# Optimization experiments

Measured on AMD Instinct MI355X. Metric: run time of the kernel, lower is better.

Reference implementation:

```python
import jax, jax.numpy as jnp
import numpy as np

STRIDES = (8.0, 16.0, 32.0)


def _decode_level(feat, W, b, stride, level):
    # feat: [bs, C, ny, nx]; W: [85, C]; b: [85]
    bs, _, ny, nx = feat.shape
    # 1x1 conv == channel contraction; output laid out as [bs, ny, nx, 85]
    p = jnp.einsum('bchw,oc->bhwo', feat, W) + b
    y = jax.nn.sigmoid(p)
    xv = jnp.arange(nx, dtype=y.dtype)            # broadcasts over last spatial dim
    yv = jnp.arange(ny, dtype=y.dtype)[:, None]   # broadcasts over row dim
    power = jnp.asarray(2.0 ** level, dtype=y.dtype)
    d = (y[..., :4] * 2.0) ** 2 * power           # dx1, dy1, dx2, dy2
    x1 = (xv + 1.0 - d[..., 0]) * stride
    y1 = (yv + 1.0 - d[..., 1]) * stride
    x2 = (xv + d[..., 2]) * stride
    y2 = (yv + d[..., 3]) * stride
    # xyxy -> xywh
    box = jnp.stack([(x1 + x2) * 0.5, (y1 + y2) * 0.5, x2 - x1, y2 - y1], axis=-1)
    out = jnp.concatenate([box, y[..., 4:]], axis=-1)  # [bs, ny, nx, 85]
    return out.reshape(bs, ny * nx, out.shape[-1])


def setup_inputs() -> dict:
    key = jax.random.key(0)
    ks = jax.random.split(key, 9)
    f32 = jnp.float32
    return {
        'x0': jax.random.normal(ks[0], (16, 256, 80, 80), dtype=f32),
        'x1': jax.random.normal(ks[1], (16, 512, 40, 40), dtype=f32),
        'x2': jax.random.normal(ks[2], (16, 1024, 20, 20), dtype=f32),
        'W0': jax.random.normal(ks[3], (85, 256), dtype=f32) * 0.05,
        'b0': jax.random.normal(ks[4], (85,), dtype=f32) * 0.05,
        'W1': jax.random.normal(ks[5], (85, 512), dtype=f32) * 0.05,
        'b1': jax.random.normal(ks[6], (85,), dtype=f32) * 0.05,
        'W2': jax.random.normal(ks[7], (85, 1024), dtype=f32) * 0.05,
        'b2': jax.random.normal(ks[8], (85,), dtype=f32) * 0.05,
    }


def reference(x0, x1, x2, W0, b0, W1, b1, W2, b2):
    feats = (x0, x1, x2)
    Ws = (W0, W1, W2)
    bs_ = (b0, b1, b2)
    z = [_decode_level(feats[i], Ws[i], bs_[i], STRIDES[i], i) for i in range(3)]
    return jnp.concatenate(z, axis=1)  # [bs, 8400, 85]
```

## Files before the change

### kernel.cpp

```cpp
#include <hip/hip_runtime.h>
#include <cstdint>


typedef __attribute__((ext_vector_type(8))) short bf16x8;
typedef __attribute__((ext_vector_type(4))) float f32x4;

constexpr int KS0 = 8, KS1 = 16, KS2 = 32;
constexpr int F0 = 6 * KS0, F1 = 6 * KS1, F2 = 6 * KS2;
constexpr int FOFF0 = 0, FOFF1 = F0, FOFF2 = F0 + F1;
constexpr int NFRAG = F0 + F1 + F2;
constexpr size_t BIAS_OFF = 0;
constexpr size_t BPK_OFF  = 1152;
constexpr size_t WS_NEED  = BPK_OFF + (size_t)NFRAG * 64 * 16;

__device__ __forceinline__ unsigned short f2bf(float f) {
    union { float f; unsigned u; } v; v.f = f;
    unsigned r = v.u + 0x7FFF + ((v.u >> 16) & 1);
    return (unsigned short)(r >> 16);
}

__global__ __launch_bounds__(256) void prep_pack(
    const float* __restrict__ W0, const float* __restrict__ W1,
    const float* __restrict__ W2,
    const float* __restrict__ b0, const float* __restrict__ b1,
    const float* __restrict__ b2,
    unsigned char* __restrict__ ws)
{
    int t = blockIdx.x * 256 + threadIdx.x;
    if (t < 288) {
        int lvl = t / 96, o = t % 96;
        const float* bp = (lvl == 0) ? b0 : (lvl == 1) ? b1 : b2;
        ((float*)(ws + BIAS_OFF))[t] = (o < 85) ? bp[o] : 0.0f;
    }
    if (t >= NFRAG * 64) return;
    int frag = t >> 6, l = t & 63;
    int C; const float* W; int f;
    if (frag < FOFF1)      { C = 256;  W = W0; f = frag;         }
    else if (frag < FOFF2) { C = 512;  W = W1; f = frag - FOFF1; }
    else                   { C = 1024; W = W2; f = frag - FOFF2; }
    int ks = f / 6, n = f % 6;
    int o  = n * 16 + (l & 15);
    int c0 = ks * 32 + (l >> 4) * 8;
    bf16x8 r;
#pragma unroll
    for (int e = 0; e < 8; ++e)
        r[e] = (o < 85) ? (short)f2bf(W[(size_t)o * C + c0 + e]) : (short)0;
    ((bf16x8*)(ws + BPK_OFF))[frag * 64 + l] = r;
}

template <int C, int HW, int NX, int LEVEL, int AOFF, int KSTEPS, int FOFF>
__device__ __forceinline__ void mfma_level(
    const float* __restrict__ feat, const unsigned char* __restrict__ ws,
    float* __restrict__ out, int blk, uint4* __restrict__ Bsm )
{
    const int tid = threadIdx.x;
    const int w   = tid >> 6;
    const int l   = tid & 63;
    const int col = l & 15;
    const int kg  = l >> 4;

    const int p0  = blk * 64 + w * 16;
    const int b   = p0 / HW;
    const int hw0 = p0 - b * HW;
    const float* fb = feat + (size_t)b * C * HW + hw0;

    const float* bias = (const float*)(ws + BIAS_OFF) + LEVEL * 96;
    const uint4* bsrc = (const uint4*)(ws + BPK_OFF) + (size_t)FOFF * 64;

    f32x4 acc[6];
#pragma unroll
    for (int n = 0; n < 6; ++n) {
        float bv = bias[n * 16 + col];
        f32x4 z = { bv, bv, bv, bv };
        acc[n] = z;
    }

    {
        const uint4* s = bsrc;
        Bsm[tid] = s[tid];
        if (tid < 128) Bsm[256 + tid] = s[256 + tid];
    }
    float fl_cur[8];
    {
        const float* p = fb + col + (size_t)(kg * 8) * HW;
#pragma unroll
        for (int e = 0; e < 8; ++e) fl_cur[e] = p[(size_t)e * HW];
    }
    __syncthreads();

    int cur = 0;
    for (int ks = 0; ks < KSTEPS; ++ks) {
        float fl_next[8];
        if (ks + 1 < KSTEPS) {
            const float* p = fb + col + (size_t)((ks + 1) * 32 + kg * 8) * HW;
#pragma unroll
            for (int e = 0; e < 8; ++e) fl_next[e] = p[(size_t)e * HW];
        }

        uint4 s0, s1;
        if (ks + 1 < KSTEPS) {
            const uint4* s = bsrc + (size_t)(ks + 1) * 384;
            s0 = s[tid];
            if (tid < 128) s1 = s[256 + tid];
        }

        bf16x8 a;
#pragma unroll
        for (int e = 0; e < 8; ++e) a[e] = (short)f2bf(fl_cur[e]);

        const bf16x8* bl = (const bf16x8*)(Bsm + (size_t)cur * 384);
#pragma unroll
        for (int n = 0; n < 6; ++n) {
            bf16x8 bq = bl[n * 64 + l];
            acc[n] = __builtin_amdgcn_mfma_f32_16x16x32_bf16(a, bq, acc[n], 0, 0, 0);
        }

        if (ks + 1 < KSTEPS) {
            uint4* d = Bsm + (size_t)(cur ^ 1) * 384;
            d[tid] = s0;
            if (tid < 128) d[256 + tid] = s1;
#pragma unroll
            for (int e = 0; e < 8; ++e) fl_cur[e] = fl_next[e];
        }
        __syncthreads();
        cur ^= 1;
    }

    constexpr float S  = (float)(8 << LEVEL);
    constexpr float P4 = 4.0f * (float)(1 << LEVEL);
#pragma unroll
    for (int j = 0; j < 4; ++j) {
        const int hw = hw0 + kg * 4 + j;
        float sg[6];
#pragma unroll
        for (int n = 0; n < 6; ++n) {
            float v = acc[n][j];
            sg[n] = __builtin_amdgcn_rcpf(1.0f + __expf(-v));
        }
        const int grp = l & 48;
        float y0 = __shfl(sg[0], grp + 0);
        float y1 = __shfl(sg[0], grp + 1);
        float y2 = __shfl(sg[0], grp + 2);
        float y3 = __shfl(sg[0], grp + 3);
        float wx = (float)(hw % NX);
        float wy = (float)(hw / NX);
        float d0 = y0 * y0 * P4, d1 = y1 * y1 * P4;
        float d2 = y2 * y2 * P4, d3 = y3 * y3 * P4;
        float x1 = (wx + 1.0f - d0) * S;
        float yA = (wy + 1.0f - d1) * S;
        float x2 = (wx + d2) * S;
        float yB = (wy + d3) * S;
        float bx = (x1 + x2) * 0.5f, by = (yA + yB) * 0.5f;
        float bw = x2 - x1,          bh = yB - yA;
        sg[0] = (col == 0) ? bx : (col == 1) ? by
              : (col == 2) ? bw : (col == 3) ? bh : sg[0];
        float* op = out + ((size_t)b * 8400 + AOFF + hw) * 85;
#pragma unroll
        for (int n = 0; n < 6; ++n) {
            int o = n * 16 + col;
            if (o < 85) op[o] = sg[n];
        }
    }
}

__global__ __launch_bounds__(256, 6) void detect_mfma(
    const float* __restrict__ x0, const float* __restrict__ x1,
    const float* __restrict__ x2,
    const unsigned char* __restrict__ ws, float* __restrict__ out)
{
    __shared__ uint4 Bsm[2 * 384];
    int blk = blockIdx.x;
    if (blk < 100)      mfma_level<1024, 400,  20, 2, 8000, KS2, FOFF2>(x2, ws, out, blk,       Bsm);
    else if (blk < 500) mfma_level<512,  1600, 40, 1, 6400, KS1, FOFF1>(x1, ws, out, blk - 100, Bsm);
    else                mfma_level<256,  6400, 80, 0, 0,    KS0, FOFF0>(x0, ws, out, blk - 500, Bsm);
}

template <int C, int HW, int NX, int LEVEL, int ONUM, bool BOX>
__device__ __forceinline__ void decode_path_fb(
    const float* __restrict__ feat, const float* __restrict__ Wm,
    const float* __restrict__ bias, float* __restrict__ out,
    int o_lo_in, int pos)
{
    const int o_lo = __builtin_amdgcn_readfirstlane(o_lo_in);
    const int b  = pos / HW;
    const int hw = pos - b * HW;
    const float* fp = feat + (size_t)b * (C * HW) + hw;
    float acc[ONUM];
#pragma unroll
    for (int j = 0; j < ONUM; ++j) acc[j] = bias[o_lo + j];
#pragma unroll 4
    for (int c = 0; c < C; ++c) {
        float fv = fp[(size_t)c * HW];
#pragma unroll
        for (int j = 0; j < ONUM; ++j)
            acc[j] = fmaf(fv, Wm[(o_lo + j) * C + c], acc[j]);
    }
#pragma unroll
    for (int j = 0; j < ONUM; ++j)
        acc[j] = __builtin_amdgcn_rcpf(1.0f + __expf(-acc[j]));
    constexpr float S = (float)(8 << LEVEL);
    constexpr int AOFF = (LEVEL == 0) ? 0 : ((LEVEL == 1) ? 6400 : 8000);
    float* op = out + ((size_t)b * 8400 + AOFF + hw) * 85 + o_lo;
    if constexpr (BOX) {
        constexpr float P4 = 4.0f * (float)(1 << LEVEL);
        float wx = (float)(hw % NX), wy = (float)(hw / NX);
        float d0 = acc[0] * acc[0] * P4, d1 = acc[1] * acc[1] * P4;
        float d2 = acc[2] * acc[2] * P4, d3 = acc[3] * acc[3] * P4;
        float x1 = (wx + 1.0f - d0) * S, y1 = (wy + 1.0f - d1) * S;
        float x2 = (wx + d2) * S,        y2 = (wy + d3) * S;
        op[0] = (x1 + x2) * 0.5f; op[1] = (y1 + y2) * 0.5f;
        op[2] = x2 - x1;          op[3] = y2 - y1;
#pragma unroll
        for (int j = 4; j < ONUM; ++j) op[j] = acc[j];
    } else {
#pragma unroll
        for (int j = 0; j < ONUM; ++j) op[j] = acc[j];
    }
}

template <int C, int HW, int NX, int LEVEL>
__device__ __forceinline__ void level_block_fb(
    const float* __restrict__ feat, const float* __restrict__ Wm,
    const float* __restrict__ bias, float* __restrict__ out, int bb)
{
    const int wave = threadIdx.x >> 6, lane = threadIdx.x & 63;
    const int pos = bb * 64 + lane;
    if      (wave == 0) decode_path_fb<C, HW, NX, LEVEL, 22, true >(feat, Wm, bias, out, 0,  pos);
    else if (wave == 1) decode_path_fb<C, HW, NX, LEVEL, 22, false>(feat, Wm, bias, out, 22, pos);
    else if (wave == 2) decode_path_fb<C, HW, NX, LEVEL, 22, false>(feat, Wm, bias, out, 44, pos);
    else                decode_path_fb<C, HW, NX, LEVEL, 19, false>(feat, Wm, bias, out, 66, pos);
}

__global__ __launch_bounds__(256) void detect_fallback(
    const float* __restrict__ x0, const float* __restrict__ x1,
    const float* __restrict__ x2,
    const float* __restrict__ w0, const float* __restrict__ w1,
    const float* __restrict__ w2,
    const float* __restrict__ b0, const float* __restrict__ b1,
    const float* __restrict__ b2, float* __restrict__ out)
{
    const int blk = blockIdx.x;
    if (blk < 100)      level_block_fb<1024, 400,  20, 2>(x2, w2, b2, out, blk);
    else if (blk < 500) level_block_fb<512,  1600, 40, 1>(x1, w1, b1, out, blk - 100);
    else                level_block_fb<256,  6400, 80, 0>(x0, w0, b0, out, blk - 500);
}

extern "C" void kernel_launch(void* const* d_in, const int* in_sizes, int n_in,
                              void* d_out, int out_size, void* d_ws, size_t ws_size,
                              hipStream_t stream)
{
    const float* x0 = (const float*)d_in[0];
    const float* x1 = (const float*)d_in[1];
    const float* x2 = (const float*)d_in[2];
    const float* W0 = (const float*)d_in[3];
    const float* b0 = (const float*)d_in[4];
    const float* W1 = (const float*)d_in[5];
    const float* b1 = (const float*)d_in[6];
    const float* W2 = (const float*)d_in[7];
    const float* b2 = (const float*)d_in[8];
    float* out = (float*)d_out;

    if (ws_size >= WS_NEED) {
        unsigned char* ws = (unsigned char*)d_ws;
        prep_pack<<<(NFRAG * 64 + 255) / 256, 256, 0, stream>>>(W0, W1, W2, b0, b1, b2, ws);
        detect_mfma<<<2100, 256, 0, stream>>>(x0, x1, x2, ws, out);
    } else {
        detect_fallback<<<2100, 256, 0, stream>>>(x0, x1, x2, W0, W1, W2, b0, b1, b2, out);
    }
}
```

Measured before the change: 47.90 us.

## Deepen weight prefetch, interleave level blocks, raise occupancy bound

```diff
diff --git a/kernel.cpp b/kernel.cpp
--- a/kernel.cpp
+++ b/kernel.cpp
@@ -58,6 +58,7 @@
     const int l   = tid & 63;
     const int col = l & 15;
     const int kg  = l >> 4;
+    const bool lo_half = (tid < 128);
 
     const int p0  = blk * 64 + w * 16;
     const int b   = p0 / HW;
@@ -78,52 +79,50 @@
     {
         const uint4* s = bsrc;
         Bsm[tid] = s[tid];
-        if (tid < 128) Bsm[256 + tid] = s[256 + tid];
-    }
-    float fl_cur[8];
+        if (lo_half) Bsm[256 + tid] = s[256 + tid];
+    }
+    float flA[8];
     {
         const float* p = fb + col + (size_t)(kg * 8) * HW;
 #pragma unroll
-        for (int e = 0; e < 8; ++e) fl_cur[e] = p[(size_t)e * HW];
+        for (int e = 0; e < 8; ++e) flA[e] = p[(size_t)e * HW];
+    }
+    uint4 pb0, pb1;
+    if (KSTEPS > 1) {
+        const uint4* s = bsrc + 384;
+        pb0 = s[tid];
+        if (lo_half) pb1 = s[256 + tid];
     }
     __syncthreads();
 
-    int cur = 0;
     for (int ks = 0; ks < KSTEPS; ++ks) {
-        float fl_next[8];
+        const int cur = ks & 1;
+
+        if (ks + 1 < KSTEPS) {
+            uint4* d = Bsm + (size_t)(cur ^ 1) * 384;
+            d[tid] = pb0;
+            if (lo_half) d[256 + tid] = pb1;
+        }
+        if (ks + 2 < KSTEPS) {
+            const uint4* s = bsrc + (size_t)(ks + 2) * 384;
+            pb0 = s[tid];
+            if (lo_half) pb1 = s[256 + tid];
+        }
+        bf16x8 a;
+#pragma unroll
+        for (int e = 0; e < 8; ++e) a[e] = (short)f2bf(flA[e]);
         if (ks + 1 < KSTEPS) {
             const float* p = fb + col + (size_t)((ks + 1) * 32 + kg * 8) * HW;
 #pragma unroll
-            for (int e = 0; e < 8; ++e) fl_next[e] = p[(size_t)e * HW];
-        }
-
-        uint4 s0, s1;
-        if (ks + 1 < KSTEPS) {
-            const uint4* s = bsrc + (size_t)(ks + 1) * 384;
-            s0 = s[tid];
-            if (tid < 128) s1 = s[256 + tid];
-        }
-
-        bf16x8 a;
-#pragma unroll
-        for (int e = 0; e < 8; ++e) a[e] = (short)f2bf(fl_cur[e]);
-
+            for (int e = 0; e < 8; ++e) flA[e] = p[(size_t)e * HW];
+        }
         const bf16x8* bl = (const bf16x8*)(Bsm + (size_t)cur * 384);
 #pragma unroll
         for (int n = 0; n < 6; ++n) {
             bf16x8 bq = bl[n * 64 + l];
             acc[n] = __builtin_amdgcn_mfma_f32_16x16x32_bf16(a, bq, acc[n], 0, 0, 0);
         }
-
-        if (ks + 1 < KSTEPS) {
-            uint4* d = Bsm + (size_t)(cur ^ 1) * 384;
-            d[tid] = s0;
-            if (tid < 128) d[256 + tid] = s1;
-#pragma unroll
-            for (int e = 0; e < 8; ++e) fl_cur[e] = fl_next[e];
-        }
         __syncthreads();
-        cur ^= 1;
     }
 
     constexpr float S  = (float)(8 << LEVEL);
@@ -163,16 +162,17 @@
     }
 }
 
-__global__ __launch_bounds__(256, 6) void detect_mfma(
+__global__ __launch_bounds__(256, 8) void detect_mfma(
     const float* __restrict__ x0, const float* __restrict__ x1,
     const float* __restrict__ x2,
     const unsigned char* __restrict__ ws, float* __restrict__ out)
 {
     __shared__ uint4 Bsm[2 * 384];
-    int blk = blockIdx.x;
-    if (blk < 100)      mfma_level<1024, 400,  20, 2, 8000, KS2, FOFF2>(x2, ws, out, blk,       Bsm);
-    else if (blk < 500) mfma_level<512,  1600, 40, 1, 6400, KS1, FOFF1>(x1, ws, out, blk - 100, Bsm);
-    else                mfma_level<256,  6400, 80, 0, 0,    KS0, FOFF0>(x0, ws, out, blk - 500, Bsm);
+    const int g = blockIdx.x / 21;
+    const int r = blockIdx.x % 21;
+    if (r == 0)      mfma_level<1024, 400,  20, 2, 8000, KS2, FOFF2>(x2, ws, out, g,               Bsm);
+    else if (r < 5)  mfma_level<512,  1600, 40, 1, 6400, KS1, FOFF1>(x1, ws, out, g * 4 + (r - 1), Bsm);
+    else             mfma_level<256,  6400, 80, 0, 0,    KS0, FOFF0>(x0, ws, out, g * 16 + (r - 5), Bsm);
 }
 
 template <int C, int HW, int NX, int LEVEL, int ONUM, bool BOX>
```

Measured after the change: 60.85 us. 1.27x slower.
